# Kernel optimization log

Measured on AMD Instinct MI355X. Metric: run time of the kernel, lower is better.

## Reference

```python
import jax, jax.numpy as jnp
import numpy as np

HIDDEN = 1024
HEADS = 16


def rotate_half(x):
    x1, x2 = jnp.split(x, 2, axis=-1)
    return jnp.concatenate((-x2, x1), axis=-1)


def rope_tables(seq_len, dim):
    inv_freq = 1.0 / 10000 ** (jnp.arange(0, dim, 2, dtype=jnp.float32) / dim)
    t = jnp.arange(seq_len, dtype=jnp.float32)
    freqs = jnp.outer(t, inv_freq)
    emb = jnp.concatenate((freqs, freqs), axis=-1)  # [S, dim]
    return jnp.cos(emb), jnp.sin(emb)


def setup_inputs() -> dict:
    key = jax.random.key(0)
    ks = jax.random.split(key, 10)
    B, S, D = 2, 2048, HIDDEN
    scale = 1.0 / np.sqrt(D)
    inp = {
        "inputs": jax.random.normal(ks[0], (B, S, D), jnp.float32),
        "context": jax.random.normal(ks[1], (B, S, D), jnp.float32),
        "Wq": jax.random.normal(ks[2], (D, D), jnp.float32) * scale,
        "bq": jnp.zeros((D,), jnp.float32),
        "Wk": jax.random.normal(ks[3], (D, D), jnp.float32) * scale,
        "bk": jnp.zeros((D,), jnp.float32),
        "Wv": jax.random.normal(ks[4], (D, D), jnp.float32) * scale,
        "bv": jnp.zeros((D,), jnp.float32),
        "Wo": jax.random.normal(ks[5], (D, D), jnp.float32) * scale,
        "bo": jnp.zeros((D,), jnp.float32),
    }
    return inp


def reference(inputs, context, Wq, bq, Wk, bk, Wv, bv, Wo, bo):
    B, S, D = inputs.shape
    H = HEADS
    hd = D // H

    q = inputs @ Wq + bq          # [B,S,D]
    k = context @ Wk + bk
    v = context @ Wv + bv

    # RoPE applied over the FULL hidden dim, pre-head-split (faithful to source).
    cos, sin = rope_tables(S, D)  # [S,D]
    # source indexes [0] after broadcasting with [1,1,S,D] tables -> effectively same values
    q = q * cos + rotate_half(q) * sin
    k = k * cos + rotate_half(k) * sin

    q = q.reshape(B, S, H, hd)
    k = k.reshape(B, S, H, hd)
    v = v.reshape(B, S, H, hd)

    # Faithful: NO transpose before attention; matmul contracts last dims of
    # q [B,S,H,hd] with k^T [B,S,hd,H] -> scores [B,S,H,H]
    scores = jnp.einsum('bshd,btd->bsht', q, jnp.zeros((1, 1, 1))) if False else None
    scores = jnp.matmul(q, jnp.swapaxes(k, -2, -1)) / jnp.sqrt(jnp.float32(hd))  # [B,S,H,H]
    attn = jax.nn.softmax(scores, axis=-1)
    ctx = jnp.matmul(attn, v)     # [B,S,H,hd]

    # source: transpose(0,2,1,3) then reshape back to (B,S,D)
    ctx = ctx.transpose(0, 2, 1, 3).reshape(B, S, D)
    out = ctx @ Wo + bo
    return out, attn
```

## Files before the change

### kernel.cpp

```cpp
#include <hip/hip_runtime.h>
#include <hip/hip_bf16.h>
#include <cstdint>

typedef __attribute__((ext_vector_type(8))) short short8;
typedef __attribute__((ext_vector_type(4))) float f32x4;
typedef __attribute__((ext_vector_type(4))) float float4v;
typedef __attribute__((ext_vector_type(4))) unsigned short us4;

#define HD 1024
#define SEQ 2048

__device__ __forceinline__ unsigned short f2bf(float f) {
  uint32_t u = __builtin_bit_cast(uint32_t, f);
  return (unsigned short)((u + 0x7FFFu + ((u >> 16) & 1u)) >> 16);
}
__device__ __forceinline__ float bf2f(unsigned short s) {
  return __builtin_bit_cast(float, (uint32_t)s << 16);
}

__device__ __forceinline__ void gload16(const unsigned short* g, unsigned short* l) {
  __builtin_amdgcn_global_load_lds(
      (const __attribute__((address_space(1))) void*)g,
      (__attribute__((address_space(3))) void*)l, 16, 0, 0);
}

__global__ __launch_bounds__(256) void prep(
    const float* __restrict__ X, const float* __restrict__ Y,
    const float* __restrict__ w0, const float* __restrict__ w1,
    const float* __restrict__ w2, const float* __restrict__ w3,
    unsigned short* __restrict__ Xh, unsigned short* __restrict__ Yh,
    unsigned short* __restrict__ wt, float* __restrict__ outz) {
  __shared__ float tile[32][33];
  int bx = blockIdx.x;
  int tid = threadIdx.x;
  if (bx < 4096) {
    const float* src = (bx >= 2048) ? Y : X;
    unsigned short* oh = (bx >= 2048) ? Yh : Xh;
    int i0 = (bx & 2047) * 512 + tid;
#pragma unroll
    for (int r = 0; r < 2; ++r) {
      int i = i0 + r * 256;
      float4v v = ((const float4v*)src)[i];
      us4 h;
#pragma unroll
      for (int j = 0; j < 4; ++j) h[j] = f2bf(v[j]);
      ((us4*)oh)[i] = h;
    }
  } else if (bx < 8192) {
    int t = bx - 4096;
    int z = t >> 10;
    int rem = t & 1023;
    int bxx = rem & 31, byy = rem >> 5;
    const float* in = (z == 0) ? w0 : (z == 1) ? w1 : (z == 2) ? w2 : w3;
    unsigned short* oh = wt + (size_t)z * 1024 * 1024;
    int tx = tid & 31, ty = tid >> 5;
    int x = bxx * 32 + tx;
    int y0 = byy * 32;
    for (int i = ty; i < 32; i += 8)
      tile[i][tx] = in[(size_t)(y0 + i) * HD + x];
    __syncthreads();
    int x2 = y0 + tx;
    int y2 = bxx * 32;
    for (int i = ty; i < 32; i += 8)
      oh[(size_t)(y2 + i) * HD + x2] = f2bf(tile[tx][i]);
  } else {
    int i0 = (bx - 8192) * 1024 + tid;
    float4v zv = {0.f, 0.f, 0.f, 0.f};
#pragma unroll
    for (int r = 0; r < 4; ++r)
      ((float4v*)outz)[i0 + r * 256] = zv;
  }
}

__global__ __launch_bounds__(256, 3) void gemm_qkv(
    const unsigned short* __restrict__ Ih, const unsigned short* __restrict__ Ch,
    const unsigned short* __restrict__ wt,
    const float* __restrict__ bq, const float* __restrict__ bk, const float* __restrict__ bv,
    unsigned short* __restrict__ qo, unsigned short* __restrict__ ko,
    unsigned short* __restrict__ vo) {
  __shared__ __align__(16) unsigned short lds[2][128][32];
  const int K = HD, N = HD;
  const size_t P = (size_t)1024 * 1024;
  int z  = blockIdx.z;
  const unsigned short* Ah = z ? Ch : Ih;
  const unsigned short* Bth = wt + (size_t)z * P;
  const float* bias = (z == 0) ? bq : (z == 1) ? bk : bv;
  unsigned short* C = (z == 0) ? qo : (z == 1) ? ko : vo;

  int m0 = blockIdx.x * 128;
  int n0 = blockIdx.y * 128;
  int tid  = threadIdx.x;
  int lane = tid & 63;
  int w    = tid >> 6;
  int quad = lane >> 4;
  int l16  = lane & 15;
  int wm = (w >> 1) * 64;
  int wn = (w & 1) * 64;

  int lr = lane >> 2;
  int g  = (lane & 3) ^ ((lr >> 1) & 3);
  const unsigned short* sp0 = Ah  + (size_t)(m0 + lr) * K + g * 8;
  const unsigned short* sp1 = Bth + (size_t)(n0 + lr) * K + g * 8;
  int s0 = w * 16;
  int s1 = (w + 4) * 16;

  f32x4 acc[4][4];
#pragma unroll
  for (int t = 0; t < 4; ++t)
#pragma unroll
    for (int u = 0; u < 4; ++u) acc[t][u] = (f32x4){0.f, 0.f, 0.f, 0.f};

  int sl8 = (quad ^ ((l16 >> 1) & 3)) * 8;

  for (int k0 = 0; k0 < K; k0 += 32) {
    __syncthreads();
    gload16(sp0 + (size_t)s0 * K + k0, &lds[0][s0][0]);
    gload16(sp0 + (size_t)s1 * K + k0, &lds[0][s1][0]);
    gload16(sp1 + (size_t)s0 * K + k0, &lds[1][s0][0]);
    gload16(sp1 + (size_t)s1 * K + k0, &lds[1][s1][0]);
    __syncthreads();

    short8 ah[4], bh[4];
#pragma unroll
    for (int t = 0; t < 4; ++t)
      ah[t] = *(const short8*)&lds[0][wm + t * 16 + l16][sl8];
#pragma unroll
    for (int u = 0; u < 4; ++u)
      bh[u] = *(const short8*)&lds[1][wn + u * 16 + l16][sl8];
#pragma unroll
    for (int t = 0; t < 4; ++t)
#pragma unroll
      for (int u = 0; u < 4; ++u)
        acc[t][u] = __builtin_amdgcn_mfma_f32_16x16x32_bf16(ah[t], bh[u], acc[t][u], 0, 0, 0);
  }

#pragma unroll
  for (int t = 0; t < 4; ++t) {
    int row = m0 + wm + t * 16 + quad * 4;
#pragma unroll
    for (int u = 0; u < 4; ++u) {
      int col = n0 + wn + u * 16 + l16;
      float bvv = bias[col];
#pragma unroll
      for (int i = 0; i < 4; ++i)
        C[(size_t)(row + i) * N + col] = f2bf(acc[t][u][i] + bvv);
    }
  }
}

__global__ __launch_bounds__(256, 3) void gemm_o_splitk(
    const unsigned short* __restrict__ Ah, const unsigned short* __restrict__ Bth,
    const float* __restrict__ bias, float* __restrict__ C) {
  __shared__ __align__(16) unsigned short lds[2][128][32];
  const int K = HD, N = HD;
  int z  = blockIdx.z;
  int m0 = blockIdx.x * 128;
  int n0 = blockIdx.y * 128;
  int tid  = threadIdx.x;
  int lane = tid & 63;
  int w    = tid >> 6;
  int quad = lane >> 4;
  int l16  = lane & 15;
  int wm = (w >> 1) * 64;
  int wn = (w & 1) * 64;

  int lr = lane >> 2;
  int g  = (lane & 3) ^ ((lr >> 1) & 3);
  const unsigned short* sp0 = Ah  + (size_t)(m0 + lr) * K + g * 8;
  const unsigned short* sp1 = Bth + (size_t)(n0 + lr) * K + g * 8;
  int s0 = w * 16;
  int s1 = (w + 4) * 16;

  f32x4 acc[4][4];
#pragma unroll
  for (int t = 0; t < 4; ++t)
#pragma unroll
    for (int u = 0; u < 4; ++u) acc[t][u] = (f32x4){0.f, 0.f, 0.f, 0.f};

  int sl8 = (quad ^ ((l16 >> 1) & 3)) * 8;

  int kend = z * 512 + 512;
  for (int k0 = z * 512; k0 < kend; k0 += 32) {
    __syncthreads();
    gload16(sp0 + (size_t)s0 * K + k0, &lds[0][s0][0]);
    gload16(sp0 + (size_t)s1 * K + k0, &lds[0][s1][0]);
    gload16(sp1 + (size_t)s0 * K + k0, &lds[1][s0][0]);
    gload16(sp1 + (size_t)s1 * K + k0, &lds[1][s1][0]);
    __syncthreads();

    short8 ah[4], bh[4];
#pragma unroll
    for (int t = 0; t < 4; ++t)
      ah[t] = *(const short8*)&lds[0][wm + t * 16 + l16][sl8];
#pragma unroll
    for (int u = 0; u < 4; ++u)
      bh[u] = *(const short8*)&lds[1][wn + u * 16 + l16][sl8];
#pragma unroll
    for (int t = 0; t < 4; ++t)
#pragma unroll
      for (int u = 0; u < 4; ++u)
        acc[t][u] = __builtin_amdgcn_mfma_f32_16x16x32_bf16(ah[t], bh[u], acc[t][u], 0, 0, 0);
  }

#pragma unroll
  for (int t = 0; t < 4; ++t) {
    int row = m0 + wm + t * 16 + quad * 4;
#pragma unroll
    for (int u = 0; u < 4; ++u) {
      int col = n0 + wn + u * 16 + l16;
      float bvv = (z == 0) ? bias[col] : 0.f;
#pragma unroll
      for (int i = 0; i < 4; ++i)
        atomicAdd(&C[(size_t)(row + i) * N + col], acc[t][u][i] + bvv);
    }
  }
}

__global__ __launch_bounds__(256) void attn_rope_k(
    const unsigned short* __restrict__ q, const unsigned short* __restrict__ kk,
    const unsigned short* __restrict__ v,
    float* __restrict__ attn_out, unsigned short* __restrict__ ctx_h) {
  __shared__ float qs[16][68], ks[16][68], vs[16][68], as[16][17];
  int m = blockIdx.x;
  int tid = threadIdx.x;
  int s = m & (SEQ - 1);
  size_t base4 = (size_t)m * (HD / 4);
  {
    int h = tid >> 4, dd = (tid & 15) * 4;
    us4 qv = ((const us4*)q)[base4 + tid];
    us4 kv = ((const us4*)kk)[base4 + tid];
    us4 vv = ((const us4*)v)[base4 + tid];
#pragma unroll
    for (int j = 0; j < 4; ++j) {
      qs[h][dd + j] = bf2f(qv[j]);
      ks[h][dd + j] = bf2f(kv[j]);
      vs[h][dd + j] = bf2f(vv[j]);
    }
  }
  __syncthreads();
#pragma unroll
  for (int d = tid; d < 512; d += 256) {
    float f = exp2f(-(float)d * 0.025952563241307517f);
    float th = (float)s * f;
    float sv, cv;
    sincosf(th, &sv, &cv);
    int h1 = d >> 6, dd = d & 63, h2 = h1 + 8;
    float q1 = qs[h1][dd], q2 = qs[h2][dd];
    qs[h1][dd] = q1 * cv - q2 * sv;
    qs[h2][dd] = q2 * cv + q1 * sv;
    float k1 = ks[h1][dd], k2 = ks[h2][dd];
    ks[h1][dd] = k1 * cv - k2 * sv;
    ks[h2][dd] = k2 * cv + k1 * sv;
  }
  __syncthreads();
  int h = tid >> 4, t = tid & 15;
  float sc = 0.f;
#pragma unroll
  for (int d = 0; d < 64; ++d) sc = fmaf(qs[h][d], ks[t][d], sc);
  sc *= 0.125f;
  float mx = sc;
  mx = fmaxf(mx, __shfl_xor(mx, 1));
  mx = fmaxf(mx, __shfl_xor(mx, 2));
  mx = fmaxf(mx, __shfl_xor(mx, 4));
  mx = fmaxf(mx, __shfl_xor(mx, 8));
  float e = expf(sc - mx);
  float sum = e;
  sum += __shfl_xor(sum, 1);
  sum += __shfl_xor(sum, 2);
  sum += __shfl_xor(sum, 4);
  sum += __shfl_xor(sum, 8);
  float a = e / sum;
  attn_out[(size_t)m * 256 + tid] = a;
  as[h][t] = a;
  __syncthreads();
  int b = m >> 11;
  for (int j = tid; j < 1024; j += 256) {
    int h2 = j >> 6, d = j & 63;
    float c = 0.f;
#pragma unroll
    for (int t2 = 0; t2 < 16; ++t2) c = fmaf(as[h2][t2], vs[t2][d], c);
    int row = b * SEQ + h2 * 128 + (s >> 4);
    int col = (s & 15) * 64 + d;
    ctx_h[(size_t)row * HD + col] = f2bf(c);
  }
}

extern "C" void kernel_launch(void* const* d_in, const int* in_sizes, int n_in,
                              void* d_out, int out_size, void* d_ws, size_t ws_size,
                              hipStream_t stream) {
  const float* inputs  = (const float*)d_in[0];
  const float* context = (const float*)d_in[1];
  const float* Wq = (const float*)d_in[2];
  const float* bq = (const float*)d_in[3];
  const float* Wk = (const float*)d_in[4];
  const float* bk = (const float*)d_in[5];
  const float* Wv = (const float*)d_in[6];
  const float* bv = (const float*)d_in[7];
  const float* Wo = (const float*)d_in[8];
  const float* bo = (const float*)d_in[9];

  float* out  = (float*)d_out;
  float* attn = out + (size_t)4096 * 1024;

  const size_t MB = 1ull << 20;
  char* wsb = (char*)d_ws;
  unsigned short* q  = (unsigned short*)(wsb + 0 * MB);
  unsigned short* k  = (unsigned short*)(wsb + 8 * MB);
  unsigned short* v  = (unsigned short*)(wsb + 16 * MB);
  unsigned short* wt = (unsigned short*)(wsb + 24 * MB);
  unsigned short* Ih = (unsigned short*)(wsb + 32 * MB);
  unsigned short* Ch = (unsigned short*)(wsb + 40 * MB);
  unsigned short* ctxh = Ih;

  prep<<<9216, 256, 0, stream>>>(inputs, context, Wq, Wk, Wv, Wo, Ih, Ch, wt, out);

  gemm_qkv<<<dim3(32, 8, 3), 256, 0, stream>>>(Ih, Ch, wt, bq, bk, bv, q, k, v);

  attn_rope_k<<<4096, 256, 0, stream>>>(q, k, v, attn, ctxh);

  const size_t P = (size_t)1024 * 1024;
  gemm_o_splitk<<<dim3(32, 8, 2), 256, 0, stream>>>(ctxh, wt + 3 * P, bo, out);
}
```

Baseline: 190.2 us.

## Double GEMM K-tile to 64 and precompute RoPE cos/sin table in prep

Both GEMM kernels now stage a 64-wide K slice per iteration instead of 32, with a new XOR swizzle for the wider LDS rows. This halves the number of barrier pairs per tile and issues two MFMA rounds per load. Separately, the prep kernel now builds a cos/sin table of size [S,512] once, and the attention kernel reads it instead of calling exp2f and sincosf for every position. The trade-off is double the LDS per block, which may lower occupancy, plus an extra 8 MB table write and read.

```diff
diff --git a/kernel.cpp b/kernel.cpp
--- a/kernel.cpp
+++ b/kernel.cpp
@@ -4,6 +4,7 @@
 
 typedef __attribute__((ext_vector_type(8))) short short8;
 typedef __attribute__((ext_vector_type(4))) float f32x4;
+typedef __attribute__((ext_vector_type(2))) float f32x2;
 typedef __attribute__((ext_vector_type(4))) float float4v;
 typedef __attribute__((ext_vector_type(4))) unsigned short us4;
 
@@ -29,7 +30,8 @@
     const float* __restrict__ w0, const float* __restrict__ w1,
     const float* __restrict__ w2, const float* __restrict__ w3,
     unsigned short* __restrict__ Xh, unsigned short* __restrict__ Yh,
-    unsigned short* __restrict__ wt, float* __restrict__ outz) {
+    unsigned short* __restrict__ wt, float* __restrict__ outz,
+    f32x2* __restrict__ tab) {
   __shared__ float tile[32][33];
   int bx = blockIdx.x;
   int tid = threadIdx.x;
@@ -63,12 +65,25 @@
     int y2 = bxx * 32;
     for (int i = ty; i < 32; i += 8)
       oh[(size_t)(y2 + i) * HD + x2] = f2bf(tile[tx][i]);
-  } else {
+  } else if (bx < 9216) {
     int i0 = (bx - 8192) * 1024 + tid;
     float4v zv = {0.f, 0.f, 0.f, 0.f};
 #pragma unroll
     for (int r = 0; r < 4; ++r)
       ((float4v*)outz)[i0 + r * 256] = zv;
+  } else {
+    int e0 = (bx - 9216) * 1024 + tid;
+#pragma unroll
+    for (int r = 0; r < 4; ++r) {
+      int e = e0 + r * 256;
+      int s = e >> 9, d = e & 511;
+      float f = exp2f(-(float)d * 0.025952563241307517f);
+      float th = (float)s * f;
+      float sv, cv;
+      sincosf(th, &sv, &cv);
+      f32x2 cs; cs[0] = cv; cs[1] = sv;
+      tab[e] = cs;
+    }
   }
 }
 
@@ -78,7 +93,7 @@
     const float* __restrict__ bq, const float* __restrict__ bk, const float* __restrict__ bv,
     unsigned short* __restrict__ qo, unsigned short* __restrict__ ko,
     unsigned short* __restrict__ vo) {
-  __shared__ __align__(16) unsigned short lds[2][128][32];
+  __shared__ __align__(16) unsigned short lds[2][128][64];
   const int K = HD, N = HD;
   const size_t P = (size_t)1024 * 1024;
   int z  = blockIdx.z;
@@ -97,12 +112,14 @@
   int wm = (w >> 1) * 64;
   int wn = (w & 1) * 64;
 
-  int lr = lane >> 2;
-  int g  = (lane & 3) ^ ((lr >> 1) & 3);
-  const unsigned short* sp0 = Ah  + (size_t)(m0 + lr) * K + g * 8;
-  const unsigned short* sp1 = Bth + (size_t)(n0 + lr) * K + g * 8;
-  int s0 = w * 16;
-  int s1 = (w + 4) * 16;
+  int ro = lane >> 3;
+  int sl = lane & 7;
+  int ge = sl ^ (ro >> 1);
+  int go = ge ^ 4;
+  const unsigned short* spA_e = Ah  + (size_t)(m0 + ro) * K + ge * 8;
+  const unsigned short* spA_o = Ah  + (size_t)(m0 + ro) * K + go * 8;
+  const unsigned short* spB_e = Bth + (size_t)(n0 + ro) * K + ge * 8;
+  const unsigned short* spB_o = Bth + (size_t)(n0 + ro) * K + go * 8;
 
   f32x4 acc[4][4];
 #pragma unroll
@@ -110,28 +127,34 @@
 #pragma unroll
     for (int u = 0; u < 4; ++u) acc[t][u] = (f32x4){0.f, 0.f, 0.f, 0.f};
 
-  int sl8 = (quad ^ ((l16 >> 1) & 3)) * 8;
-
-  for (int k0 = 0; k0 < K; k0 += 32) {
-    __syncthreads();
-    gload16(sp0 + (size_t)s0 * K + k0, &lds[0][s0][0]);
-    gload16(sp0 + (size_t)s1 * K + k0, &lds[0][s1][0]);
-    gload16(sp1 + (size_t)s0 * K + k0, &lds[1][s0][0]);
-    gload16(sp1 + (size_t)s1 * K + k0, &lds[1][s1][0]);
-    __syncthreads();
-
-    short8 ah[4], bh[4];
-#pragma unroll
-    for (int t = 0; t < 4; ++t)
-      ah[t] = *(const short8*)&lds[0][wm + t * 16 + l16][sl8];
-#pragma unroll
-    for (int u = 0; u < 4; ++u)
-      bh[u] = *(const short8*)&lds[1][wn + u * 16 + l16][sl8];
-#pragma unroll
-    for (int t = 0; t < 4; ++t)
+  for (int k0 = 0; k0 < K; k0 += 64) {
+    __syncthreads();
+#pragma unroll
+    for (int i = 0; i < 4; ++i) {
+      int seg = w + i * 4;
+      const unsigned short* pa = (seg & 1) ? spA_o : spA_e;
+      const unsigned short* pb = (seg & 1) ? spB_o : spB_e;
+      gload16(pa + (size_t)seg * 8 * K + k0, &lds[0][seg * 8][0]);
+      gload16(pb + (size_t)seg * 8 * K + k0, &lds[1][seg * 8][0]);
+    }
+    __syncthreads();
+
+#pragma unroll
+    for (int j = 0; j < 2; ++j) {
+      int sl8 = (((j << 2) | quad) ^ (l16 >> 1)) * 8;
+      short8 ah[4], bh[4];
+#pragma unroll
+      for (int t = 0; t < 4; ++t)
+        ah[t] = *(const short8*)&lds[0][wm + t * 16 + l16][sl8];
 #pragma unroll
       for (int u = 0; u < 4; ++u)
-        acc[t][u] = __builtin_amdgcn_mfma_f32_16x16x32_bf16(ah[t], bh[u], acc[t][u], 0, 0, 0);
+        bh[u] = *(const short8*)&lds[1][wn + u * 16 + l16][sl8];
+#pragma unroll
+      for (int t = 0; t < 4; ++t)
+#pragma unroll
+        for (int u = 0; u < 4; ++u)
+          acc[t][u] = __builtin_amdgcn_mfma_f32_16x16x32_bf16(ah[t], bh[u], acc[t][u], 0, 0, 0);
+    }
   }
 
 #pragma unroll
@@ -151,7 +174,7 @@
 __global__ __launch_bounds__(256, 3) void gemm_o_splitk(
     const unsigned short* __restrict__ Ah, const unsigned short* __restrict__ Bth,
     const float* __restrict__ bias, float* __restrict__ C) {
-  __shared__ __align__(16) unsigned short lds[2][128][32];
+  __shared__ __align__(16) unsigned short lds[2][128][64];
   const int K = HD, N = HD;
   int z  = blockIdx.z;
   int m0 = blockIdx.x * 128;
@@ -164,12 +187,14 @@
   int wm = (w >> 1) * 64;
   int wn = (w & 1) * 64;
 
-  int lr = lane >> 2;
-  int g  = (lane & 3) ^ ((lr >> 1) & 3);
-  const unsigned short* sp0 = Ah  + (size_t)(m0 + lr) * K + g * 8;
-  const unsigned short* sp1 = Bth + (size_t)(n0 + lr) * K + g * 8;
-  int s0 = w * 16;
-  int s1 = (w + 4) * 16;
+  int ro = lane >> 3;
+  int sl = lane & 7;
+  int ge = sl ^ (ro >> 1);
+  int go = ge ^ 4;
+  const unsigned short* spA_e = Ah  + (size_t)(m0 + ro) * K + ge * 8;
+  const unsigned short* spA_o = Ah  + (size_t)(m0 + ro) * K + go * 8;
+  const unsigned short* spB_e = Bth + (size_t)(n0 + ro) * K + ge * 8;
+  const unsigned short* spB_o = Bth + (size_t)(n0 + ro) * K + go * 8;
 
   f32x4 acc[4][4];
 #pragma unroll
@@ -177,29 +202,35 @@
 #pragma unroll
     for (int u = 0; u < 4; ++u) acc[t][u] = (f32x4){0.f, 0.f, 0.f, 0.f};
 
-  int sl8 = (quad ^ ((l16 >> 1) & 3)) * 8;
-
   int kend = z * 512 + 512;
-  for (int k0 = z * 512; k0 < kend; k0 += 32) {
-    __syncthreads();
-    gload16(sp0 + (size_t)s0 * K + k0, &lds[0][s0][0]);
-    gload16(sp0 + (size_t)s1 * K + k0, &lds[0][s1][0]);
-    gload16(sp1 + (size_t)s0 * K + k0, &lds[1][s0][0]);
-    gload16(sp1 + (size_t)s1 * K + k0, &lds[1][s1][0]);
-    __syncthreads();
-
-    short8 ah[4], bh[4];
-#pragma unroll
-    for (int t = 0; t < 4; ++t)
-      ah[t] = *(const short8*)&lds[0][wm + t * 16 + l16][sl8];
-#pragma unroll
-    for (int u = 0; u < 4; ++u)
-      bh[u] = *(const short8*)&lds[1][wn + u * 16 + l16][sl8];
-#pragma unroll
-    for (int t = 0; t < 4; ++t)
+  for (int k0 = z * 512; k0 < kend; k0 += 64) {
+    __syncthreads();
+#pragma unroll
+    for (int i = 0; i < 4; ++i) {
+      int seg = w + i * 4;
+      const unsigned short* pa = (seg & 1) ? spA_o : spA_e;
+      const unsigned short* pb = (seg & 1) ? spB_o : spB_e;
+      gload16(pa + (size_t)seg * 8 * K + k0, &lds[0][seg * 8][0]);
+      gload16(pb + (size_t)seg * 8 * K + k0, &lds[1][seg * 8][0]);
+    }
+    __syncthreads();
+
+#pragma unroll
+    for (int j = 0; j < 2; ++j) {
+      int sl8 = (((j << 2) | quad) ^ (l16 >> 1)) * 8;
+      short8 ah[4], bh[4];
+#pragma unroll
+      for (int t = 0; t < 4; ++t)
+        ah[t] = *(const short8*)&lds[0][wm + t * 16 + l16][sl8];
 #pragma unroll
       for (int u = 0; u < 4; ++u)
-        acc[t][u] = __builtin_amdgcn_mfma_f32_16x16x32_bf16(ah[t], bh[u], acc[t][u], 0, 0, 0);
+        bh[u] = *(const short8*)&lds[1][wn + u * 16 + l16][sl8];
+#pragma unroll
+      for (int t = 0; t < 4; ++t)
+#pragma unroll
+        for (int u = 0; u < 4; ++u)
+          acc[t][u] = __builtin_amdgcn_mfma_f32_16x16x32_bf16(ah[t], bh[u], acc[t][u], 0, 0, 0);
+    }
   }
 
 #pragma unroll
@@ -218,7 +249,7 @@
 
 __global__ __launch_bounds__(256) void attn_rope_k(
     const unsigned short* __restrict__ q, const unsigned short* __restrict__ kk,
-    const unsigned short* __restrict__ v,
+    const unsigned short* __restrict__ v, const f32x2* __restrict__ tab,
     float* __restrict__ attn_out, unsigned short* __restrict__ ctx_h) {
   __shared__ float qs[16][68], ks[16][68], vs[16][68], as[16][17];
   int m = blockIdx.x;
@@ -240,10 +271,8 @@
   __syncthreads();
 #pragma unroll
   for (int d = tid; d < 512; d += 256) {
-    float f = exp2f(-(float)d * 0.025952563241307517f);
-    float th = (float)s * f;
-    float sv, cv;
-    sincosf(th, &sv, &cv);
+    f32x2 cs = tab[(s << 9) + d];
+    float cv = cs[0], sv = cs[1];
     int h1 = d >> 6, dd = d & 63, h2 = h1 + 8;
     float q1 = qs[h1][dd], q2 = qs[h2][dd];
     qs[h1][dd] = q1 * cv - q2 * sv;
@@ -310,13 +339,15 @@
   unsigned short* wt = (unsigned short*)(wsb + 24 * MB);
   unsigned short* Ih = (unsigned short*)(wsb + 32 * MB);
   unsigned short* Ch = (unsigned short*)(wsb + 40 * MB);
+  f32x2* tab = (f32x2*)(wsb + 48 * MB);
   unsigned short* ctxh = Ih;
 
-  prep<<<9216, 256, 0, stream>>>(inputs, context, Wq, Wk, Wv, Wo, Ih, Ch, wt, out);
+  prep<<<10240, 256, 0, stream>>>(inputs, context, Wq, Wk, Wv, Wo,
+                                  Ih, Ch, wt, out, tab);
 
   gemm_qkv<<<dim3(32, 8, 3), 256, 0, stream>>>(Ih, Ch, wt, bq, bk, bv, q, k, v);
 
-  attn_rope_k<<<4096, 256, 0, stream>>>(q, k, v, attn, ctxh);
+  attn_rope_k<<<4096, 256, 0, stream>>>(q, k, v, tab, attn, ctxh);
 
   const size_t P = (size_t)1024 * 1024;
   gemm_o_splitk<<<dim3(32, 8, 2), 256, 0, stream>>>(ctxh, wt + 3 * P, bo, out);
```

Result: no change. 189.4 us (-0.5%).
